# Optimization experiments

Measured on AMD Instinct MI355X. Metric: run time of the kernel, lower is better.

The kernel has to match this reference:

```python
import jax, jax.numpy as jnp
import numpy as np

B, H, W, D, C = 2, 16, 16, 16, 128
UNITS = 128
BN_EPS = 1e-3  # keras BatchNormalization default epsilon


def setup_inputs() -> dict:
    key = jax.random.key(0)
    ks = jax.random.split(key, 12)
    lim = np.sqrt(3.0 / C)  # VarianceScaling(1.0, fan_avg, uniform)
    inp = {
        "x": jax.random.normal(ks[0], (B, H, W, D, C), dtype=jnp.float32),
        "gamma": jnp.ones((C,), jnp.float32),
        "beta": jnp.zeros((C,), jnp.float32),
        "moving_mean": jax.random.normal(ks[1], (C,), jnp.float32) * 0.1,
        "moving_var": jnp.ones((C,), jnp.float32) + 0.1 * jax.random.uniform(ks[2], (C,)),
        "Wq": jax.random.uniform(ks[3], (C, UNITS), jnp.float32, -lim, lim),
        "bq": jnp.zeros((UNITS,), jnp.float32),
        "Wk": jax.random.uniform(ks[4], (C, UNITS), jnp.float32, -lim, lim),
        "bk": jnp.zeros((UNITS,), jnp.float32),
        "Wv": jax.random.uniform(ks[5], (C, UNITS), jnp.float32, -lim, lim),
        "bv": jnp.zeros((UNITS,), jnp.float32),
        # proj uses kernel_init(0.0) -> effectively ~0; use tiny scale to keep grads nonzero
        "Wp": jax.random.uniform(ks[6], (UNITS, UNITS), jnp.float32, -1e-5, 1e-5),
        "bp": jnp.zeros((UNITS,), jnp.float32),
    }
    return inp


def reference(x, gamma, beta, moving_mean, moving_var, Wq, bq, Wk, bk, Wv, bv, Wp, bp):
    # BatchNormalization (inference mode): per-channel affine normalization
    xn = (x - moving_mean) * jax.lax.rsqrt(moving_var + BN_EPS) * gamma + beta
    b, h, w, d, c = xn.shape
    n = h * w * d
    scale = jnp.asarray(UNITS, jnp.float32) ** -0.5
    q = (xn @ Wq + bq).reshape(b, n, UNITS)
    k = (xn @ Wk + bk).reshape(b, n, UNITS)
    v = (xn @ Wv + bv).reshape(b, n, UNITS)
    # full self-attention over flattened 3D spatial dims: [b, n, n] scores
    attn = jax.nn.softmax(jnp.einsum('bnc,bmc->bnm', q, k) * scale, axis=-1)
    proj = jnp.einsum('bnm,bmc->bnc', attn, v).reshape(b, h, w, d, UNITS)
    proj = proj @ Wp + bp
    return xn + proj
```

## Files before the change

### kernel.cpp

```cpp
#include <hip/hip_runtime.h>
#include <hip/hip_bf16.h>

using bh8     = __attribute__((ext_vector_type(8))) short;
using floatx4 = __attribute__((ext_vector_type(4))) float;

#define MFMA16 __builtin_amdgcn_mfma_f32_16x16x32_bf16

__device__ __forceinline__ float b2f(short s) {
    union { unsigned u; float f; } v; v.u = ((unsigned)(unsigned short)s) << 16; return v.f;
}
__device__ __forceinline__ short f2b(float f) {
    union { float f; unsigned u; } v; v.f = f;
    unsigned r = (v.u + 0x7fffu + ((v.u >> 16) & 1u)) >> 16;
    return (short)r;
}
__device__ __forceinline__ float ldf(const void* p, int i, bool f32) {
    return f32 ? ((const float*)p)[i] : b2f(((const short*)p)[i]);
}
__device__ __forceinline__ bool detect_f32(const void* gamma) {
    return ((*(const unsigned*)gamma) & 0xFFFFu) == 0u;
}
__device__ __forceinline__ void gl2lds16(const short* g, short* l) {
    __builtin_amdgcn_global_load_lds(
        (const __attribute__((address_space(1))) void*)g,
        (__attribute__((address_space(3))) void*)l, 16, 0, 0);
}

#define LDW 136

__global__ __launch_bounds__(256) void k_bn_qkv(
    const void* __restrict__ xp,
    const void* __restrict__ gp, const void* __restrict__ bep,
    const void* __restrict__ mmp, const void* __restrict__ mvp,
    const void* __restrict__ Wqp, const void* __restrict__ bqp,
    const void* __restrict__ Wkp, const void* __restrict__ bkp,
    const void* __restrict__ Wvp, const void* __restrict__ bvp,
    short* __restrict__ Qo, short* __restrict__ Ko, short* __restrict__ Vt)
{
    __shared__ float sS[128], sT[128];
    __shared__ __align__(16) short Wt[128 * LDW];
    const bool f32 = detect_f32(gp);
    const int tid = threadIdx.x, wave = tid >> 6, lane = tid & 63;
    const int lq = lane >> 4, lr = lane & 15;
    const int g = blockIdx.x >> 8;
    const int tile = blockIdx.x & 255;
    const int qrow = tile * 32 + (wave >> 1) * 16;
    const int u0 = (wave & 1) * 64;

    if (tid < 128) {
        float ga = ldf(gp, tid, f32), be = ldf(bep, tid, f32);
        float mm = ldf(mmp, tid, f32), mv = ldf(mvp, tid, f32);
        float s = ga * rsqrtf(mv + 1e-3f);
        sS[tid] = s;
        sT[tid] = be - mm * s;
    }

    const void* W  = (g == 0) ? Wqp : ((g == 1) ? Wkp : Wvp);
    const void* bb = (g == 0) ? bqp : ((g == 1) ? bkp : bvp);

    if (f32) {
        for (int it = 0; it < 16; ++it) {
            int f = (it * 256 + tid) * 4;
            int c = f >> 7, u = f & 127;
            floatx4 wv = *(const floatx4*)((const float*)W + f);
            #pragma unroll
            for (int jj = 0; jj < 4; ++jj) {
                int j = (jj + (tid >> 1)) & 3;
                Wt[(u + j) * LDW + c] = f2b(wv[j]);
            }
        }
    } else {
        for (int it = 0; it < 8; ++it) {
            int f = (it * 256 + tid) * 8;
            int c = f >> 7, u = f & 127;
            bh8 wv = *(const bh8*)((const short*)W + f);
            #pragma unroll
            for (int jj = 0; jj < 8; ++jj) {
                int j = (jj + tid) & 7;
                Wt[(u + j) * LDW + c] = wv[j];
            }
        }
    }
    __syncthreads();

    bh8 a[4];
    #pragma unroll
    for (int ks = 0; ks < 4; ++ks) {
        int c0 = ks * 32 + lq * 8;
        floatx4 s0 = *(const floatx4*)(&sS[c0]), s1 = *(const floatx4*)(&sS[c0 + 4]);
        floatx4 t0 = *(const floatx4*)(&sT[c0]), t1 = *(const floatx4*)(&sT[c0 + 4]);
        bh8 af;
        if (f32) {
            const float* xr = (const float*)xp + (size_t)(qrow + lr) * 128 + c0;
            floatx4 x0 = *(const floatx4*)xr, x1 = *(const floatx4*)(xr + 4);
            #pragma unroll
            for (int j = 0; j < 4; ++j) {
                af[j]     = f2b(x0[j] * s0[j] + t0[j]);
                af[j + 4] = f2b(x1[j] * s1[j] + t1[j]);
            }
        } else {
            bh8 xv = *(const bh8*)((const short*)xp + (size_t)(qrow + lr) * 128 + c0);
            #pragma unroll
            for (int j = 0; j < 4; ++j) {
                af[j]     = f2b(b2f(xv[j]) * s0[j] + t0[j]);
                af[j + 4] = f2b(b2f(xv[j + 4]) * s1[j] + t1[j]);
            }
        }
        a[ks] = af;
    }

    floatx4 acc[4] = {};
    #pragma unroll
    for (int ks = 0; ks < 4; ++ks)
        #pragma unroll
        for (int t = 0; t < 4; ++t) {
            bh8 b = *(const bh8*)(&Wt[(u0 + t * 16 + lr) * LDW + ks * 32 + lq * 8]);
            acc[t] = MFMA16(a[ks], b, acc[t], 0, 0, 0);
        }

    if (g < 2) {
        #pragma unroll
        for (int t = 0; t < 4; ++t) {
            int u = u0 + t * 16 + lr;
            float bias = ldf(bb, u, f32);
            #pragma unroll
            for (int r = 0; r < 4; ++r) {
                int grow = qrow + lq * 4 + r;
                short vb = f2b(acc[t][r] + bias);
                if (g == 0) Qo[(size_t)grow * 128 + u] = vb;
                else        Ko[(size_t)grow * 128 + u] = vb;
            }
        }
    } else {
        __syncthreads();
        short* sVt = Wt;
        #pragma unroll
        for (int t = 0; t < 4; ++t) {
            int u = u0 + t * 16 + lr;
            float bias = ldf(bb, u, f32);
            #pragma unroll
            for (int r = 0; r < 4; ++r) {
                int n = (wave >> 1) * 16 + lq * 4 + r;
                sVt[u * 40 + n] = f2b(acc[t][r] + bias);
            }
        }
        __syncthreads();
        int u = tid >> 1, nh = tid & 1;
        int n0g = tile * 32;
        int bsb = n0g >> 12, nn = (n0g & 4095) + nh * 16;
        bh8 v0 = *(const bh8*)(&sVt[u * 40 + nh * 16]);
        bh8 v1 = *(const bh8*)(&sVt[u * 40 + nh * 16 + 8]);
        short* dst = Vt + (size_t)bsb * 128 * 4096 + (size_t)u * 4096 + nn;
        *(bh8*)dst = v0;
        *(bh8*)(dst + 8) = v1;
    }
}

__global__ __launch_bounds__(256, 2) void k_attn(
    const short* __restrict__ Qg, const short* __restrict__ Kg,
    const short* __restrict__ Vtg, short* __restrict__ Op,
    float* __restrict__ Lq)
{
    __shared__ __align__(16) short sK[2][64 * 128];
    __shared__ __align__(16) short sV[2][128 * 64];
    __shared__ __align__(16) short sP[4][16 * 64];

    const int tid = threadIdx.x, wave = tid >> 6, lane = tid & 63;
    const int lq = lane >> 4, lr = lane & 15;
    const int qt = blockIdx.x >> 2, kq = blockIdx.x & 3;
    const int mq = qt * 64, bs = mq >> 12, key0q = kq * 1024;
    const short* Kb = Kg + (size_t)bs * 4096 * 128;
    const short* Vb = Vtg + (size_t)bs * 128 * 4096;
    const int qrow = mq + wave * 16;

    bh8 aq[4];
    #pragma unroll
    for (int ks = 0; ks < 4; ++ks)
        aq[ks] = *(const bh8*)(Qg + (size_t)(qrow + lr) * 128 + ks * 32 + lq * 8);

    const int kKeyB = wave * 16 + (lane >> 4), kCh = lane & 15;
    const int vUB   = wave * 32 + (lane >> 3), vCh = lane & 7;

    floatx4 accO[8] = {};
    float lsum[4] = {0.f, 0.f, 0.f, 0.f};
    const float c2 = 0.12751743f;
    const float m2 = 11.541560f;
    short* Pw = &sP[wave][0];

    #pragma unroll
    for (int rd = 0; rd < 4; ++rd) {
        int key = kKeyB + rd * 4;
        gl2lds16(Kb + (size_t)(key0q + key) * 128 + ((kCh ^ (key & 7)) << 3),
                 &sK[0][(wave * 16 + rd * 4) * 128]);
    }
    #pragma unroll
    for (int rd = 0; rd < 4; ++rd) {
        int u = vUB + rd * 8;
        gl2lds16(Vb + (size_t)u * 4096 + key0q + ((vCh ^ (u & 7)) << 3),
                 &sV[0][(wave * 32 + rd * 8) * 64]);
    }
    __syncthreads();

    for (int it = 0; it < 16; ++it) {
        const int p = it & 1;
        if (it < 15) {
            const int key1 = key0q + (it + 1) * 64;
            #pragma unroll
            for (int rd = 0; rd < 4; ++rd) {
                int key = kKeyB + rd * 4;
                gl2lds16(Kb + (size_t)(key1 + key) * 128 + ((kCh ^ (key & 7)) << 3),
                         &sK[p ^ 1][(wave * 16 + rd * 4) * 128]);
            }
            #pragma unroll
            for (int rd = 0; rd < 4; ++rd) {
                int u = vUB + rd * 8;
                gl2lds16(Vb + (size_t)u * 4096 + key1 + ((vCh ^ (u & 7)) << 3),
                         &sV[p ^ 1][(wave * 32 + rd * 8) * 64]);
            }
        }

        const short* sKp = &sK[p][0];
        const short* sVp = &sV[p][0];

        floatx4 s[4];
        #pragma unroll
        for (int t = 0; t < 4; ++t) {
            floatx4 acc = {};
            #pragma unroll
            for (int ks = 0; ks < 4; ++ks) {
                bh8 b = *(const bh8*)(&sKp[(t * 16 + lr) * 128 +
                                           (((ks * 4 + lq) ^ (lr & 7)) << 3)]);
                acc = MFMA16(aq[ks], b, acc, 0, 0, 0);
            }
            s[t] = acc;
        }
        #pragma unroll
        for (int t = 0; t < 4; ++t)
            #pragma unroll
            for (int r = 0; r < 4; ++r)
                s[t][r] = exp2f(fmaf(s[t][r], c2, -m2));
        #pragma unroll
        for (int r = 0; r < 4; ++r)
            lsum[r] += (s[0][r] + s[1][r]) + (s[2][r] + s[3][r]);

        #pragma unroll
        for (int t = 0; t < 4; ++t)
            #pragma unroll
            for (int r = 0; r < 4; ++r)
                Pw[(lq * 4 + r) * 64 + (((t ^ lq) << 4) + lr)] = f2b(s[t][r]);

        bh8 ap0 = *(const bh8*)(&Pw[lr * 64 + (((lq >> 1) ^ (lr >> 2)) << 4) + ((lq & 1) << 3)]);
        bh8 ap1 = *(const bh8*)(&Pw[lr * 64 + (((2 + (lq >> 1)) ^ (lr >> 2)) << 4) + ((lq & 1) << 3)]);

        #pragma unroll
        for (int t = 0; t < 8; ++t) {
            bh8 b0 = *(const bh8*)(&sVp[(t * 16 + lr) * 64 + ((lq ^ (lr & 7)) << 3)]);
            bh8 b1 = *(const bh8*)(&sVp[(t * 16 + lr) * 64 + (((4 + lq) ^ (lr & 7)) << 3)]);
            accO[t] = MFMA16(ap0, b0, accO[t], 0, 0, 0);
            accO[t] = MFMA16(ap1, b1, accO[t], 0, 0, 0);
        }
        if (it < 15) __syncthreads();
    }

    #pragma unroll
    for (int r = 0; r < 4; ++r) {
        float v = lsum[r];
        v += __shfl_xor(v, 1, 16);
        v += __shfl_xor(v, 2, 16);
        v += __shfl_xor(v, 4, 16);
        v += __shfl_xor(v, 8, 16);
        lsum[r] = v;
    }
    if (lr == 0) {
        #pragma unroll
        for (int r = 0; r < 4; ++r)
            Lq[(size_t)kq * 8192 + qrow + lq * 4 + r] = lsum[r];
    }
    short* Ob = Op + (size_t)kq * 8192 * 128;
    #pragma unroll
    for (int t = 0; t < 8; ++t)
        #pragma unroll
        for (int r = 0; r < 4; ++r)
            Ob[(size_t)(qrow + lq * 4 + r) * 128 + t * 16 + lr] = f2b(accO[t][r]);
}

__global__ __launch_bounds__(256) void k_proj(
    const short* __restrict__ Op, const float* __restrict__ Lq,
    const void* __restrict__ Wpp, const void* __restrict__ bpp,
    const void* __restrict__ xp,
    const void* __restrict__ gp, const void* __restrict__ bep,
    const void* __restrict__ mmp, const void* __restrict__ mvp,
    void* __restrict__ outp)
{
    __shared__ float sS[128], sT[128];
    __shared__ __align__(16) short Wt[64 * LDW];
    __shared__ __align__(16) short sO[32 * LDW];
    const bool f32 = detect_f32(gp);
    const int tid = threadIdx.x, wave = tid >> 6, lane = tid & 63;
    const int lq = lane >> 4, lr = lane & 15;
    const int uh = blockIdx.x & 1;
    const int tile = blockIdx.x >> 1;
    const int row0 = tile * 32;
    const int rh = wave >> 1, us = wave & 1;

    if (tid < 128) {
        float ga = ldf(gp, tid, f32), be = ldf(bep, tid, f32);
        float mm = ldf(mmp, tid, f32), mv = ldf(mvp, tid, f32);
        float s = ga * rsqrtf(mv + 1e-3f);
        sS[tid] = s;
        sT[tid] = be - mm * s;
    }

    if (f32) {
        for (int it = 0; it < 8; ++it) {
            int f = (it * 256 + tid) * 4;
            int c = f >> 6, ul = f & 63;
            floatx4 wv = *(const floatx4*)((const float*)Wpp + (size_t)c * 128 + uh * 64 + ul);
            #pragma unroll
            for (int jj = 0; jj < 4; ++jj) {
                int j = (jj + (tid >> 1)) & 3;
                Wt[(ul + j) * LDW + c] = f2b(wv[j]);
            }
        }
    } else {
        for (int it = 0; it < 4; ++it) {
            int f = (it * 256 + tid) * 8;
            int c = f >> 6, ul = f & 63;
            bh8 wv = *(const bh8*)((const short*)Wpp + (size_t)c * 128 + uh * 64 + ul);
            #pragma unroll
            for (int jj = 0; jj < 8; ++jj) {
                int j = (jj + tid) & 7;
                Wt[(ul + j) * LDW + c] = wv[j];
            }
        }
    }

    #pragma unroll
    for (int e = 0; e < 2; ++e) {
        int f = (e * 256 + tid) * 8;
        int row = f >> 7, c = f & 127;
        int grow = row0 + row;
        float L = Lq[grow] + Lq[8192 + grow] + Lq[16384 + grow] + Lq[24576 + grow];
        float invL = 1.0f / L;
        float sum[8] = {};
        #pragma unroll
        for (int w = 0; w < 4; ++w) {
            bh8 p = *(const bh8*)(Op + (size_t)w * 8192 * 128 + (size_t)grow * 128 + c);
            #pragma unroll
            for (int j = 0; j < 8; ++j) sum[j] += b2f(p[j]);
        }
        bh8 o;
        #pragma unroll
        for (int j = 0; j < 8; ++j) o[j] = f2b(sum[j] * invL);
        *(bh8*)(&sO[row * LDW + c]) = o;
    }
    __syncthreads();

    bh8 a[4];
    #pragma unroll
    for (int ks = 0; ks < 4; ++ks)
        a[ks] = *(const bh8*)(&sO[(rh * 16 + lr) * LDW + ks * 32 + lq * 8]);

    floatx4 acc[2] = {};
    #pragma unroll
    for (int ks = 0; ks < 4; ++ks)
        #pragma unroll
        for (int t = 0; t < 2; ++t) {
            bh8 b = *(const bh8*)(&Wt[(us * 32 + t * 16 + lr) * LDW + ks * 32 + lq * 8]);
            acc[t] = MFMA16(a[ks], b, acc[t], 0, 0, 0);
        }

    #pragma unroll
    for (int t = 0; t < 2; ++t) {
        int u = uh * 64 + us * 32 + t * 16 + lr;
        float bias = ldf(bpp, u, f32);
        float su = sS[u], tu = sT[u];
        #pragma unroll
        for (int r = 0; r < 4; ++r) {
            int grow = row0 + rh * 16 + lq * 4 + r;
            float xnv = ldf(xp, grow * 128 + u, f32) * su + tu;
            float v = acc[t][r] + bias + xnv;
            size_t idx = (size_t)grow * 128 + u;
            if (f32) ((float*)outp)[idx] = v;
            else     ((short*)outp)[idx] = f2b(v);
        }
    }
}

extern "C" void kernel_launch(void* const* d_in, const int* in_sizes, int n_in,
                              void* d_out, int out_size, void* d_ws, size_t ws_size,
                              hipStream_t stream)
{
    const void* x     = d_in[0];
    const void* gamma = d_in[1];
    const void* beta  = d_in[2];
    const void* mmean = d_in[3];
    const void* mvar  = d_in[4];
    const void* Wq    = d_in[5];
    const void* bq    = d_in[6];
    const void* Wk    = d_in[7];
    const void* bk    = d_in[8];
    const void* Wv    = d_in[9];
    const void* bv    = d_in[10];
    const void* Wp    = d_in[11];
    const void* bp    = d_in[12];

    char* ws = (char*)d_ws;
    const size_t MB = 1024u * 1024u;
    short* Q     = (short*)(ws + 0 * MB);
    short* K     = (short*)(ws + 2 * MB);
    short* Vt    = (short*)(ws + 4 * MB);
    short* Opart = (short*)(ws + 6 * MB);
    float* Lsum  = (float*)(ws + 14 * MB);

    k_bn_qkv<<<768, 256, 0, stream>>>(x, gamma, beta, mmean, mvar,
                                      Wq, bq, Wk, bk, Wv, bv, Q, K, Vt);
    k_attn<<<512, 256, 0, stream>>>(Q, K, Vt, Opart, Lsum);
    k_proj<<<512, 256, 0, stream>>>(Opart, Lsum, Wp, bp, x,
                                    gamma, beta, mmean, mvar, d_out);
}
```

Measured before the change: 133.1 us.

## Pre-transpose weights once and retile attention to 32 query rows per wave

Adds a small kernel that converts and transposes all four weight matrices to bf16 once, so the QKV and projection kernels read B fragments straight from global memory instead of rebuilding a transposed copy in LDS in every block. The attention kernel now gives each wave 32 query rows and splits keys 8 ways with 32-key tiles, so each K and V fragment feeds two MFMAs, with smaller LDS buffers. The projection reduction now sums 8 partials instead of 4, which doubles its partial-output traffic and adds one more kernel launch.

Measured after the change: 139.3 us. 1.05x slower.

```diff
diff --git a/kernel.cpp b/kernel.cpp
--- a/kernel.cpp
+++ b/kernel.cpp
@@ -26,19 +26,58 @@
         (__attribute__((address_space(3))) void*)l, 16, 0, 0);
 }
 
-#define LDW 136
+#define TLD 136
+__global__ __launch_bounds__(256) void k_wT(
+    const void* __restrict__ W0, const void* __restrict__ W1,
+    const void* __restrict__ W2, const void* __restrict__ W3,
+    short* __restrict__ WT, const void* __restrict__ gp)
+{
+    __shared__ __align__(16) short T[128 * TLD];
+    const bool f32 = detect_f32(gp);
+    const void* W = (blockIdx.x == 0) ? W0 : (blockIdx.x == 1) ? W1
+                   : (blockIdx.x == 2) ? W2 : W3;
+    const int tid = threadIdx.x;
+
+    for (int it = 0; it < 8; ++it) {
+        int f = (it * 256 + tid) * 8;
+        int c = f >> 7, u = f & 127;
+        short v[8];
+        if (f32) {
+            floatx4 a = *(const floatx4*)((const float*)W + f);
+            floatx4 b = *(const floatx4*)((const float*)W + f + 4);
+            #pragma unroll
+            for (int j = 0; j < 4; ++j) { v[j] = f2b(a[j]); v[j + 4] = f2b(b[j]); }
+        } else {
+            bh8 a = *(const bh8*)((const short*)W + f);
+            #pragma unroll
+            for (int j = 0; j < 8; ++j) v[j] = a[j];
+        }
+        #pragma unroll
+        for (int jj = 0; jj < 8; ++jj) {
+            int j = (jj + tid) & 7;
+            T[(u + j) * TLD + c] = v[j];
+        }
+    }
+    __syncthreads();
+    short* WTd = WT + blockIdx.x * 16384;
+    for (int it = 0; it < 8; ++it) {
+        int f = (it * 256 + tid) * 8;
+        int u = f >> 7, c = f & 127;
+        *(bh8*)(WTd + u * 128 + c) = *(const bh8*)(&T[u * TLD + c]);
+    }
+}
 
 __global__ __launch_bounds__(256) void k_bn_qkv(
     const void* __restrict__ xp,
     const void* __restrict__ gp, const void* __restrict__ bep,
     const void* __restrict__ mmp, const void* __restrict__ mvp,
-    const void* __restrict__ Wqp, const void* __restrict__ bqp,
-    const void* __restrict__ Wkp, const void* __restrict__ bkp,
-    const void* __restrict__ Wvp, const void* __restrict__ bvp,
+    const short* __restrict__ WT,
+    const void* __restrict__ bqp, const void* __restrict__ bkp,
+    const void* __restrict__ bvp,
     short* __restrict__ Qo, short* __restrict__ Ko, short* __restrict__ Vt)
 {
     __shared__ float sS[128], sT[128];
-    __shared__ __align__(16) short Wt[128 * LDW];
+    __shared__ __align__(16) short sVt[128 * 40];
     const bool f32 = detect_f32(gp);
     const int tid = threadIdx.x, wave = tid >> 6, lane = tid & 63;
     const int lq = lane >> 4, lr = lane & 15;
@@ -53,33 +92,6 @@
         float s = ga * rsqrtf(mv + 1e-3f);
         sS[tid] = s;
         sT[tid] = be - mm * s;
-    }
-
-    const void* W  = (g == 0) ? Wqp : ((g == 1) ? Wkp : Wvp);
-    const void* bb = (g == 0) ? bqp : ((g == 1) ? bkp : bvp);
-
-    if (f32) {
-        for (int it = 0; it < 16; ++it) {
-            int f = (it * 256 + tid) * 4;
-            int c = f >> 7, u = f & 127;
-            floatx4 wv = *(const floatx4*)((const float*)W + f);
-            #pragma unroll
-            for (int jj = 0; jj < 4; ++jj) {
-                int j = (jj + (tid >> 1)) & 3;
-                Wt[(u + j) * LDW + c] = f2b(wv[j]);
-            }
-        }
-    } else {
-        for (int it = 0; it < 8; ++it) {
-            int f = (it * 256 + tid) * 8;
-            int c = f >> 7, u = f & 127;
-            bh8 wv = *(const bh8*)((const short*)W + f);
-            #pragma unroll
-            for (int jj = 0; jj < 8; ++jj) {
-                int j = (jj + tid) & 7;
-                Wt[(u + j) * LDW + c] = wv[j];
-            }
-        }
     }
     __syncthreads();
 
@@ -109,12 +121,15 @@
         a[ks] = af;
     }
 
+    const short* WTg = WT + g * 16384;
+    const void* bb = (g == 0) ? bqp : ((g == 1) ? bkp : bvp);
+
     floatx4 acc[4] = {};
     #pragma unroll
     for (int ks = 0; ks < 4; ++ks)
         #pragma unroll
         for (int t = 0; t < 4; ++t) {
-            bh8 b = *(const bh8*)(&Wt[(u0 + t * 16 + lr) * LDW + ks * 32 + lq * 8]);
+            bh8 b = *(const bh8*)(WTg + (size_t)(u0 + t * 16 + lr) * 128 + ks * 32 + lq * 8);
             acc[t] = MFMA16(a[ks], b, acc[t], 0, 0, 0);
         }
 
@@ -132,8 +147,6 @@
             }
         }
     } else {
-        __syncthreads();
-        short* sVt = Wt;
         #pragma unroll
         for (int t = 0; t < 4; ++t) {
             int u = u0 + t * 16 + lr;
@@ -161,140 +174,160 @@
     const short* __restrict__ Vtg, short* __restrict__ Op,
     float* __restrict__ Lq)
 {
-    __shared__ __align__(16) short sK[2][64 * 128];
-    __shared__ __align__(16) short sV[2][128 * 64];
-    __shared__ __align__(16) short sP[4][16 * 64];
+    __shared__ __align__(16) short sK[2][32 * 128];
+    __shared__ __align__(16) short sV[2][128 * 32];
+    __shared__ __align__(16) short sP[4][32 * 40];
 
     const int tid = threadIdx.x, wave = tid >> 6, lane = tid & 63;
     const int lq = lane >> 4, lr = lane & 15;
-    const int qt = blockIdx.x >> 2, kq = blockIdx.x & 3;
-    const int mq = qt * 64, bs = mq >> 12, key0q = kq * 1024;
+    const int qt = blockIdx.x >> 3, kq = blockIdx.x & 7;
+    const int mq = qt * 128, bs = mq >> 12, key0q = kq * 512;
     const short* Kb = Kg + (size_t)bs * 4096 * 128;
     const short* Vb = Vtg + (size_t)bs * 128 * 4096;
-    const int qrow = mq + wave * 16;
-
-    bh8 aq[4];
-    #pragma unroll
-    for (int ks = 0; ks < 4; ++ks)
-        aq[ks] = *(const bh8*)(Qg + (size_t)(qrow + lr) * 128 + ks * 32 + lq * 8);
-
-    const int kKeyB = wave * 16 + (lane >> 4), kCh = lane & 15;
-    const int vUB   = wave * 32 + (lane >> 3), vCh = lane & 7;
-
-    floatx4 accO[8] = {};
-    float lsum[4] = {0.f, 0.f, 0.f, 0.f};
+    const int qrow0 = mq + wave * 32;
+
+    bh8 aq[2][4];
+    #pragma unroll
+    for (int rt = 0; rt < 2; ++rt)
+        #pragma unroll
+        for (int ks = 0; ks < 4; ++ks)
+            aq[rt][ks] = *(const bh8*)(Qg + (size_t)(qrow0 + rt * 16 + lr) * 128 + ks * 32 + lq * 8);
+
+    const int kKey = lane >> 4, kCh = lane & 15;
+    const int vU   = lane >> 2, vCh = lane & 3;
+
+    floatx4 accO[2][8] = {};
+    float lsum[2][4] = {};
     const float c2 = 0.12751743f;
     const float m2 = 11.541560f;
     short* Pw = &sP[wave][0];
 
     #pragma unroll
-    for (int rd = 0; rd < 4; ++rd) {
-        int key = kKeyB + rd * 4;
+    for (int rd = 0; rd < 2; ++rd) {
+        int key = wave * 8 + rd * 4 + kKey;
         gl2lds16(Kb + (size_t)(key0q + key) * 128 + ((kCh ^ (key & 7)) << 3),
-                 &sK[0][(wave * 16 + rd * 4) * 128]);
-    }
-    #pragma unroll
-    for (int rd = 0; rd < 4; ++rd) {
-        int u = vUB + rd * 8;
-        gl2lds16(Vb + (size_t)u * 4096 + key0q + ((vCh ^ (u & 7)) << 3),
-                 &sV[0][(wave * 32 + rd * 8) * 64]);
+                 &sK[0][(wave * 8 + rd * 4) * 128]);
+    }
+    #pragma unroll
+    for (int rd = 0; rd < 2; ++rd) {
+        int u = wave * 32 + rd * 16 + vU;
+        gl2lds16(Vb + (size_t)u * 4096 + key0q + ((vCh ^ (u & 3)) << 3),
+                 &sV[0][(wave * 32 + rd * 16) * 32]);
     }
     __syncthreads();
 
     for (int it = 0; it < 16; ++it) {
         const int p = it & 1;
         if (it < 15) {
-            const int key1 = key0q + (it + 1) * 64;
-            #pragma unroll
-            for (int rd = 0; rd < 4; ++rd) {
-                int key = kKeyB + rd * 4;
+            const int key1 = key0q + (it + 1) * 32;
+            #pragma unroll
+            for (int rd = 0; rd < 2; ++rd) {
+                int key = wave * 8 + rd * 4 + kKey;
                 gl2lds16(Kb + (size_t)(key1 + key) * 128 + ((kCh ^ (key & 7)) << 3),
-                         &sK[p ^ 1][(wave * 16 + rd * 4) * 128]);
-            }
-            #pragma unroll
-            for (int rd = 0; rd < 4; ++rd) {
-                int u = vUB + rd * 8;
-                gl2lds16(Vb + (size_t)u * 4096 + key1 + ((vCh ^ (u & 7)) << 3),
-                         &sV[p ^ 1][(wave * 32 + rd * 8) * 64]);
+                         &sK[p ^ 1][(wave * 8 + rd * 4) * 128]);
+            }
+            #pragma unroll
+            for (int rd = 0; rd < 2; ++rd) {
+                int u = wave * 32 + rd * 16 + vU;
+                gl2lds16(Vb + (size_t)u * 4096 + key1 + ((vCh ^ (u & 3)) << 3),
+                         &sV[p ^ 1][(wave * 32 + rd * 16) * 32]);
             }
         }
 
         const short* sKp = &sK[p][0];
         const short* sVp = &sV[p][0];
 
-        floatx4 s[4];
-        #pragma unroll
-        for (int t = 0; t < 4; ++t) {
-            floatx4 acc = {};
+        floatx4 s[2][2];
+        #pragma unroll
+        for (int rt = 0; rt < 2; ++rt)
+            #pragma unroll
+            for (int t = 0; t < 2; ++t)
+                s[rt][t] = floatx4{};
+        #pragma unroll
+        for (int t = 0; t < 2; ++t)
             #pragma unroll
             for (int ks = 0; ks < 4; ++ks) {
                 bh8 b = *(const bh8*)(&sKp[(t * 16 + lr) * 128 +
                                            (((ks * 4 + lq) ^ (lr & 7)) << 3)]);
-                acc = MFMA16(aq[ks], b, acc, 0, 0, 0);
-            }
-            s[t] = acc;
-        }
-        #pragma unroll
-        for (int t = 0; t < 4; ++t)
+                #pragma unroll
+                for (int rt = 0; rt < 2; ++rt)
+                    s[rt][t] = MFMA16(aq[rt][ks], b, s[rt][t], 0, 0, 0);
+            }
+
+        #pragma unroll
+        for (int rt = 0; rt < 2; ++rt)
+            #pragma unroll
+            for (int t = 0; t < 2; ++t)
+                #pragma unroll
+                for (int r = 0; r < 4; ++r) {
+                    float e = exp2f(fmaf(s[rt][t][r], c2, -m2));
+                    s[rt][t][r] = e;
+                    lsum[rt][r] += e;
+                }
+
+        #pragma unroll
+        for (int rt = 0; rt < 2; ++rt)
+            #pragma unroll
+            for (int t = 0; t < 2; ++t)
+                #pragma unroll
+                for (int r = 0; r < 4; ++r)
+                    Pw[(rt * 16 + lq * 4 + r) * 40 + t * 16 + lr] = f2b(s[rt][t][r]);
+
+        bh8 ap[2];
+        #pragma unroll
+        for (int rt = 0; rt < 2; ++rt)
+            ap[rt] = *(const bh8*)(&Pw[(rt * 16 + lr) * 40 + lq * 8]);
+
+        #pragma unroll
+        for (int t = 0; t < 8; ++t) {
+            int u = t * 16 + lr;
+            bh8 b = *(const bh8*)(&sVp[u * 32 + ((lq ^ (lr & 3)) << 3)]);
+            #pragma unroll
+            for (int rt = 0; rt < 2; ++rt)
+                accO[rt][t] = MFMA16(ap[rt], b, accO[rt][t], 0, 0, 0);
+        }
+        if (it < 15) __syncthreads();
+    }
+
+    #pragma unroll
+    for (int rt = 0; rt < 2; ++rt)
+        #pragma unroll
+        for (int r = 0; r < 4; ++r) {
+            float v = lsum[rt][r];
+            v += __shfl_xor(v, 1, 16);
+            v += __shfl_xor(v, 2, 16);
+            v += __shfl_xor(v, 4, 16);
+            v += __shfl_xor(v, 8, 16);
+            lsum[rt][r] = v;
+        }
+    if (lr == 0) {
+        #pragma unroll
+        for (int rt = 0; rt < 2; ++rt)
             #pragma unroll
             for (int r = 0; r < 4; ++r)
-                s[t][r] = exp2f(fmaf(s[t][r], c2, -m2));
-        #pragma unroll
-        for (int r = 0; r < 4; ++r)
-            lsum[r] += (s[0][r] + s[1][r]) + (s[2][r] + s[3][r]);
-
-        #pragma unroll
-        for (int t = 0; t < 4; ++t)
+                Lq[(size_t)kq * 8192 + qrow0 + rt * 16 + lq * 4 + r] = lsum[rt][r];
+    }
+    short* Ob = Op + (size_t)kq * 8192 * 128;
+    #pragma unroll
+    for (int rt = 0; rt < 2; ++rt)
+        #pragma unroll
+        for (int t = 0; t < 8; ++t)
             #pragma unroll
             for (int r = 0; r < 4; ++r)
-                Pw[(lq * 4 + r) * 64 + (((t ^ lq) << 4) + lr)] = f2b(s[t][r]);
-
-        bh8 ap0 = *(const bh8*)(&Pw[lr * 64 + (((lq >> 1) ^ (lr >> 2)) << 4) + ((lq & 1) << 3)]);
-        bh8 ap1 = *(const bh8*)(&Pw[lr * 64 + (((2 + (lq >> 1)) ^ (lr >> 2)) << 4) + ((lq & 1) << 3)]);
-
-        #pragma unroll
-        for (int t = 0; t < 8; ++t) {
-            bh8 b0 = *(const bh8*)(&sVp[(t * 16 + lr) * 64 + ((lq ^ (lr & 7)) << 3)]);
-            bh8 b1 = *(const bh8*)(&sVp[(t * 16 + lr) * 64 + (((4 + lq) ^ (lr & 7)) << 3)]);
-            accO[t] = MFMA16(ap0, b0, accO[t], 0, 0, 0);
-            accO[t] = MFMA16(ap1, b1, accO[t], 0, 0, 0);
-        }
-        if (it < 15) __syncthreads();
-    }
-
-    #pragma unroll
-    for (int r = 0; r < 4; ++r) {
-        float v = lsum[r];
-        v += __shfl_xor(v, 1, 16);
-        v += __shfl_xor(v, 2, 16);
-        v += __shfl_xor(v, 4, 16);
-        v += __shfl_xor(v, 8, 16);
-        lsum[r] = v;
-    }
-    if (lr == 0) {
-        #pragma unroll
-        for (int r = 0; r < 4; ++r)
-            Lq[(size_t)kq * 8192 + qrow + lq * 4 + r] = lsum[r];
-    }
-    short* Ob = Op + (size_t)kq * 8192 * 128;
-    #pragma unroll
-    for (int t = 0; t < 8; ++t)
-        #pragma unroll
-        for (int r = 0; r < 4; ++r)
-            Ob[(size_t)(qrow + lq * 4 + r) * 128 + t * 16 + lr] = f2b(accO[t][r]);
+                Ob[(size_t)(qrow0 + rt * 16 + lq * 4 + r) * 128 + t * 16 + lr]
+                    = f2b(accO[rt][t][r]);
 }
 
 __global__ __launch_bounds__(256) void k_proj(
     const short* __restrict__ Op, const float* __restrict__ Lq,
-    const void* __restrict__ Wpp, const void* __restrict__ bpp,
+    const short* __restrict__ WpT, const void* __restrict__ bpp,
     const void* __restrict__ xp,
     const void* __restrict__ gp, const void* __restrict__ bep,
     const void* __restrict__ mmp, const void* __restrict__ mvp,
     void* __restrict__ outp)
 {
     __shared__ float sS[128], sT[128];
-    __shared__ __align__(16) short Wt[64 * LDW];
-    __shared__ __align__(16) short sO[32 * LDW];
+    __shared__ __align__(16) short sO[32 * 136];
     const bool f32 = detect_f32(gp);
     const int tid = threadIdx.x, wave = tid >> 6, lane = tid & 63;
     const int lq = lane >> 4, lr = lane & 15;
@@ -311,40 +344,18 @@
         sT[tid] = be - mm * s;
     }
 
-    if (f32) {
-        for (int it = 0; it < 8; ++it) {
-            int f = (it * 256 + tid) * 4;
-            int c = f >> 6, ul = f & 63;
-            floatx4 wv = *(const floatx4*)((const float*)Wpp + (size_t)c * 128 + uh * 64 + ul);
-            #pragma unroll
-            for (int jj = 0; jj < 4; ++jj) {
-                int j = (jj + (tid >> 1)) & 3;
-                Wt[(ul + j) * LDW + c] = f2b(wv[j]);
-            }
-        }
-    } else {
-        for (int it = 0; it < 4; ++it) {
-            int f = (it * 256 + tid) * 8;
-            int c = f >> 6, ul = f & 63;
-            bh8 wv = *(const bh8*)((const short*)Wpp + (size_t)c * 128 + uh * 64 + ul);
-            #pragma unroll
-            for (int jj = 0; jj < 8; ++jj) {
-                int j = (jj + tid) & 7;
-                Wt[(ul + j) * LDW + c] = wv[j];
-            }
-        }
-    }
-
     #pragma unroll
     for (int e = 0; e < 2; ++e) {
         int f = (e * 256 + tid) * 8;
         int row = f >> 7, c = f & 127;
         int grow = row0 + row;
-        float L = Lq[grow] + Lq[8192 + grow] + Lq[16384 + grow] + Lq[24576 + grow];
+        float L = 0.f;
+        #pragma unroll
+        for (int w = 0; w < 8; ++w) L += Lq[(size_t)w * 8192 + grow];
         float invL = 1.0f / L;
         float sum[8] = {};
         #pragma unroll
-        for (int w = 0; w < 4; ++w) {
+        for (int w = 0; w < 8; ++w) {
             bh8 p = *(const bh8*)(Op + (size_t)w * 8192 * 128 + (size_t)grow * 128 + c);
             #pragma unroll
             for (int j = 0; j < 8; ++j) sum[j] += b2f(p[j]);
@@ -352,21 +363,22 @@
         bh8 o;
         #pragma unroll
         for (int j = 0; j < 8; ++j) o[j] = f2b(sum[j] * invL);
-        *(bh8*)(&sO[row * LDW + c]) = o;
+        *(bh8*)(&sO[row * 136 + c]) = o;
     }
     __syncthreads();
 
     bh8 a[4];
     #pragma unroll
     for (int ks = 0; ks < 4; ++ks)
-        a[ks] = *(const bh8*)(&sO[(rh * 16 + lr) * LDW + ks * 32 + lq * 8]);
+        a[ks] = *(const bh8*)(&sO[(rh * 16 + lr) * 136 + ks * 32 + lq * 8]);
 
     floatx4 acc[2] = {};
     #pragma unroll
     for (int ks = 0; ks < 4; ++ks)
         #pragma unroll
         for (int t = 0; t < 2; ++t) {
-            bh8 b = *(const bh8*)(&Wt[(us * 32 + t * 16 + lr) * LDW + ks * 32 + lq * 8]);
+            bh8 b = *(const bh8*)(WpT + (size_t)(uh * 64 + us * 32 + t * 16 + lr) * 128
+                                       + ks * 32 + lq * 8);
             acc[t] = MFMA16(a[ks], b, acc[t], 0, 0, 0);
         }
 
@@ -407,15 +419,17 @@
 
     char* ws = (char*)d_ws;
     const size_t MB = 1024u * 1024u;
-    short* Q     = (short*)(ws + 0 * MB);
-    short* K     = (short*)(ws + 2 * MB);
-    short* Vt    = (short*)(ws + 4 * MB);
-    short* Opart = (short*)(ws + 6 * MB);
-    float* Lsum  = (float*)(ws + 14 * MB);
-
+    short* WT    = (short*)(ws + 0 * MB);
+    short* Q     = (short*)(ws + 1 * MB);
+    short* K     = (short*)(ws + 3 * MB);
+    short* Vt    = (short*)(ws + 5 * MB);
+    short* Opart = (short*)(ws + 7 * MB);
+    float* Lsum  = (float*)(ws + 23 * MB);
+
+    k_wT<<<4, 256, 0, stream>>>(Wq, Wk, Wv, Wp, WT, gamma);
     k_bn_qkv<<<768, 256, 0, stream>>>(x, gamma, beta, mmean, mvar,
-                                      Wq, bq, Wk, bk, Wv, bv, Q, K, Vt);
+                                      WT, bq, bk, bv, Q, K, Vt);
     k_attn<<<512, 256, 0, stream>>>(Q, K, Vt, Opart, Lsum);
-    k_proj<<<512, 256, 0, stream>>>(Opart, Lsum, Wp, bp, x,
+    k_proj<<<512, 256, 0, stream>>>(Opart, Lsum, WT + 3 * 16384, bp, x,
                                     gamma, beta, mmean, mvar, d_out);
 }
```

## Use two-wave attention blocks with 32-row query tiles per wave and 32-key steps

Applied to the files above, without the earlier changes.

The attention kernel moves from four waves of 16 query rows each to two waves that each handle 32 query rows (two MFMA row tiles). Each K and V fragment read from LDS is then reused across both row tiles. The key tile per iteration shrinks from 64 to 32 and the loop runs 32 times. LDS footprint drops and the P buffer uses a padded stride instead of an XOR swizzle. In exchange there are more barriers per block, fewer waves per block, and more accumulator registers per thread.

New measurement: 156.7 us. 17.7% more time.

```diff
diff --git a/kernel.cpp b/kernel.cpp
--- a/kernel.cpp
+++ b/kernel.cpp
@@ -156,14 +156,16 @@
     }
 }
 
-__global__ __launch_bounds__(256, 2) void k_attn(
+#define PLDA 40
+
+__global__ __launch_bounds__(128, 2) void k_attn(
     const short* __restrict__ Qg, const short* __restrict__ Kg,
     const short* __restrict__ Vtg, short* __restrict__ Op,
     float* __restrict__ Lq)
 {
-    __shared__ __align__(16) short sK[2][64 * 128];
-    __shared__ __align__(16) short sV[2][128 * 64];
-    __shared__ __align__(16) short sP[4][16 * 64];
+    __shared__ __align__(16) short sK[2][32 * 128];
+    __shared__ __align__(16) short sV[2][128 * 32];
+    __shared__ __align__(16) short sP[2][32 * PLDA];
 
     const int tid = threadIdx.x, wave = tid >> 6, lane = tid & 63;
     const int lq = lane >> 4, lr = lane & 15;
@@ -171,117 +173,138 @@
     const int mq = qt * 64, bs = mq >> 12, key0q = kq * 1024;
     const short* Kb = Kg + (size_t)bs * 4096 * 128;
     const short* Vb = Vtg + (size_t)bs * 128 * 4096;
-    const int qrow = mq + wave * 16;
-
-    bh8 aq[4];
-    #pragma unroll
-    for (int ks = 0; ks < 4; ++ks)
-        aq[ks] = *(const bh8*)(Qg + (size_t)(qrow + lr) * 128 + ks * 32 + lq * 8);
-
-    const int kKeyB = wave * 16 + (lane >> 4), kCh = lane & 15;
-    const int vUB   = wave * 32 + (lane >> 3), vCh = lane & 7;
-
-    floatx4 accO[8] = {};
-    float lsum[4] = {0.f, 0.f, 0.f, 0.f};
+    const int qrow0 = mq + wave * 32;
+
+    bh8 aq[2][4];
+    #pragma unroll
+    for (int rt = 0; rt < 2; ++rt)
+        #pragma unroll
+        for (int ks = 0; ks < 4; ++ks)
+            aq[rt][ks] = *(const bh8*)(Qg + (size_t)(qrow0 + rt * 16 + lr) * 128 + ks * 32 + lq * 8);
+
+    const int kKey = lane >> 4, kCh = lane & 15;
+    const int vU   = lane >> 2, vCh = lane & 3;
+
+    floatx4 accO[2][8] = {};
+    float lsum[2][4] = {};
     const float c2 = 0.12751743f;
     const float m2 = 11.541560f;
     short* Pw = &sP[wave][0];
 
     #pragma unroll
     for (int rd = 0; rd < 4; ++rd) {
-        int key = kKeyB + rd * 4;
+        int key = wave * 16 + rd * 4 + kKey;
         gl2lds16(Kb + (size_t)(key0q + key) * 128 + ((kCh ^ (key & 7)) << 3),
                  &sK[0][(wave * 16 + rd * 4) * 128]);
     }
     #pragma unroll
     for (int rd = 0; rd < 4; ++rd) {
-        int u = vUB + rd * 8;
-        gl2lds16(Vb + (size_t)u * 4096 + key0q + ((vCh ^ (u & 7)) << 3),
-                 &sV[0][(wave * 32 + rd * 8) * 64]);
+        int u = wave * 64 + rd * 16 + vU;
+        gl2lds16(Vb + (size_t)u * 4096 + key0q + ((vCh ^ ((u >> 1) & 3)) << 3),
+                 &sV[0][(wave * 64 + rd * 16) * 32]);
     }
     __syncthreads();
 
-    for (int it = 0; it < 16; ++it) {
+    for (int it = 0; it < 32; ++it) {
         const int p = it & 1;
-        if (it < 15) {
-            const int key1 = key0q + (it + 1) * 64;
+        if (it < 31) {
+            const int key1 = key0q + (it + 1) * 32;
             #pragma unroll
             for (int rd = 0; rd < 4; ++rd) {
-                int key = kKeyB + rd * 4;
+                int key = wave * 16 + rd * 4 + kKey;
                 gl2lds16(Kb + (size_t)(key1 + key) * 128 + ((kCh ^ (key & 7)) << 3),
                          &sK[p ^ 1][(wave * 16 + rd * 4) * 128]);
             }
             #pragma unroll
             for (int rd = 0; rd < 4; ++rd) {
-                int u = vUB + rd * 8;
-                gl2lds16(Vb + (size_t)u * 4096 + key1 + ((vCh ^ (u & 7)) << 3),
-                         &sV[p ^ 1][(wave * 32 + rd * 8) * 64]);
+                int u = wave * 64 + rd * 16 + vU;
+                gl2lds16(Vb + (size_t)u * 4096 + key1 + ((vCh ^ ((u >> 1) & 3)) << 3),
+                         &sV[p ^ 1][(wave * 64 + rd * 16) * 32]);
             }
         }
 
         const short* sKp = &sK[p][0];
         const short* sVp = &sV[p][0];
 
-        floatx4 s[4];
-        #pragma unroll
-        for (int t = 0; t < 4; ++t) {
-            floatx4 acc = {};
+        floatx4 s[2][2];
+        #pragma unroll
+        for (int rt = 0; rt < 2; ++rt)
+            #pragma unroll
+            for (int t = 0; t < 2; ++t)
+                s[rt][t] = floatx4{};
+        #pragma unroll
+        for (int t = 0; t < 2; ++t)
             #pragma unroll
             for (int ks = 0; ks < 4; ++ks) {
                 bh8 b = *(const bh8*)(&sKp[(t * 16 + lr) * 128 +
                                            (((ks * 4 + lq) ^ (lr & 7)) << 3)]);
-                acc = MFMA16(aq[ks], b, acc, 0, 0, 0);
-            }
-            s[t] = acc;
-        }
-        #pragma unroll
-        for (int t = 0; t < 4; ++t)
+                #pragma unroll
+                for (int rt = 0; rt < 2; ++rt)
+                    s[rt][t] = MFMA16(aq[rt][ks], b, s[rt][t], 0, 0, 0);
+            }
+
+        #pragma unroll
+        for (int rt = 0; rt < 2; ++rt)
+            #pragma unroll
+            for (int t = 0; t < 2; ++t)
+                #pragma unroll
+                for (int r = 0; r < 4; ++r) {
+                    float e = exp2f(fmaf(s[rt][t][r], c2, -m2));
+                    s[rt][t][r] = e;
+                    lsum[rt][r] += e;
+                }
+
+        #pragma unroll
+        for (int rt = 0; rt < 2; ++rt)
+            #pragma unroll
+            for (int t = 0; t < 2; ++t)
+                #pragma unroll
+                for (int r = 0; r < 4; ++r)
+                    Pw[(rt * 16 + lq * 4 + r) * PLDA + t * 16 + lr] = f2b(s[rt][t][r]);
+
+        bh8 ap[2];
+        #pragma unroll
+        for (int rt = 0; rt < 2; ++rt)
+            ap[rt] = *(const bh8*)(&Pw[(rt * 16 + lr) * PLDA + lq * 8]);
+
+        #pragma unroll
+        for (int t = 0; t < 8; ++t) {
+            int u = t * 16 + lr;
+            bh8 b = *(const bh8*)(&sVp[u * 32 + ((lq ^ ((lr >> 1) & 3)) << 3)]);
+            #pragma unroll
+            for (int rt = 0; rt < 2; ++rt)
+                accO[rt][t] = MFMA16(ap[rt], b, accO[rt][t], 0, 0, 0);
+        }
+        if (it < 31) __syncthreads();
+    }
+
+    #pragma unroll
+    for (int rt = 0; rt < 2; ++rt)
+        #pragma unroll
+        for (int r = 0; r < 4; ++r) {
+            float v = lsum[rt][r];
+            v += __shfl_xor(v, 1, 16);
+            v += __shfl_xor(v, 2, 16);
+            v += __shfl_xor(v, 4, 16);
+            v += __shfl_xor(v, 8, 16);
+            lsum[rt][r] = v;
+        }
+    if (lr == 0) {
+        #pragma unroll
+        for (int rt = 0; rt < 2; ++rt)
             #pragma unroll
             for (int r = 0; r < 4; ++r)
-                s[t][r] = exp2f(fmaf(s[t][r], c2, -m2));
-        #pragma unroll
-        for (int r = 0; r < 4; ++r)
-            lsum[r] += (s[0][r] + s[1][r]) + (s[2][r] + s[3][r]);
-
-        #pragma unroll
-        for (int t = 0; t < 4; ++t)
+                Lq[(size_t)kq * 8192 + qrow0 + rt * 16 + lq * 4 + r] = lsum[rt][r];
+    }
+    short* Ob = Op + (size_t)kq * 8192 * 128;
+    #pragma unroll
+    for (int rt = 0; rt < 2; ++rt)
+        #pragma unroll
+        for (int t = 0; t < 8; ++t)
             #pragma unroll
             for (int r = 0; r < 4; ++r)
-                Pw[(lq * 4 + r) * 64 + (((t ^ lq) << 4) + lr)] = f2b(s[t][r]);
-
-        bh8 ap0 = *(const bh8*)(&Pw[lr * 64 + (((lq >> 1) ^ (lr >> 2)) << 4) + ((lq & 1) << 3)]);
-        bh8 ap1 = *(const bh8*)(&Pw[lr * 64 + (((2 + (lq >> 1)) ^ (lr >> 2)) << 4) + ((lq & 1) << 3)]);
-
-        #pragma unroll
-        for (int t = 0; t < 8; ++t) {
-            bh8 b0 = *(const bh8*)(&sVp[(t * 16 + lr) * 64 + ((lq ^ (lr & 7)) << 3)]);
-            bh8 b1 = *(const bh8*)(&sVp[(t * 16 + lr) * 64 + (((4 + lq) ^ (lr & 7)) << 3)]);
-            accO[t] = MFMA16(ap0, b0, accO[t], 0, 0, 0);
-            accO[t] = MFMA16(ap1, b1, accO[t], 0, 0, 0);
-        }
-        if (it < 15) __syncthreads();
-    }
-
-    #pragma unroll
-    for (int r = 0; r < 4; ++r) {
-        float v = lsum[r];
-        v += __shfl_xor(v, 1, 16);
-        v += __shfl_xor(v, 2, 16);
-        v += __shfl_xor(v, 4, 16);
-        v += __shfl_xor(v, 8, 16);
-        lsum[r] = v;
-    }
-    if (lr == 0) {
-        #pragma unroll
-        for (int r = 0; r < 4; ++r)
-            Lq[(size_t)kq * 8192 + qrow + lq * 4 + r] = lsum[r];
-    }
-    short* Ob = Op + (size_t)kq * 8192 * 128;
-    #pragma unroll
-    for (int t = 0; t < 8; ++t)
-        #pragma unroll
-        for (int r = 0; r < 4; ++r)
-            Ob[(size_t)(qrow + lq * 4 + r) * 128 + t * 16 + lr] = f2b(accO[t][r]);
+                Ob[(size_t)(qrow0 + rt * 16 + lq * 4 + r) * 128 + t * 16 + lr]
+                    = f2b(accO[rt][t][r]);
 }
 
 __global__ __launch_bounds__(256) void k_proj(
@@ -415,7 +438,7 @@
 
     k_bn_qkv<<<768, 256, 0, stream>>>(x, gamma, beta, mmean, mvar,
                                       Wq, bq, Wk, bk, Wv, bv, Q, K, Vt);
-    k_attn<<<512, 256, 0, stream>>>(Q, K, Vt, Opart, Lsum);
+    k_attn<<<512, 128, 0, stream>>>(Q, K, Vt, Opart, Lsum);
     k_proj<<<512, 256, 0, stream>>>(Opart, Lsum, Wp, bp, x,
                                     gamma, beta, mmean, mvar, d_out);
 }
```
